# Optimization experiments

Hardware: AMD Instinct MI355X
Metric: run time of the kernel (lower is better)

Reference implementation:

```python
import jax, jax.numpy as jnp
import numpy as np

H = 16  # hidden/input size
EPS = 1e-5


def _lstm_layer(xs, W_ih, W_hh, b_ih, b_hh):
    """xs: [T, B, in]. Returns (ys [T,B,H], h_final [B,H]). PyTorch gate order i,f,g,o."""
    B = xs.shape[1]
    h0 = jnp.zeros((B, H), xs.dtype)
    c0 = jnp.zeros((B, H), xs.dtype)
    bias = b_ih + b_hh  # [4H]

    def step(carry, x_t):
        h, c = carry
        gates = x_t @ W_ih.T + h @ W_hh.T + bias  # [B, 4H]
        i, f, g, o = jnp.split(gates, 4, axis=-1)
        i = jax.nn.sigmoid(i)
        f = jax.nn.sigmoid(f)
        g = jnp.tanh(g)
        o = jax.nn.sigmoid(o)
        c = f * c + i * g
        h = o * jnp.tanh(c)
        return (h, c), h

    (h_fin, _), ys = jax.lax.scan(step, (h0, c0), xs)
    return ys, h_fin


def setup_inputs() -> dict:
    key = jax.random.key(0)
    ks = jax.random.split(key, 12)
    s = 1.0 / np.sqrt(H)  # PyTorch LSTM/Linear init scale
    B, T = 4096, 512
    x = jax.random.normal(ks[0], (B, T, H), dtype=jnp.float32)
    u = lambda k, shp: jax.random.uniform(k, shp, jnp.float32, -s, s)
    return {
        "x": x,
        "W_ih0": u(ks[1], (4 * H, H)), "W_hh0": u(ks[2], (4 * H, H)),
        "b_ih0": u(ks[3], (4 * H,)), "b_hh0": u(ks[4], (4 * H,)),
        "W_ih1": u(ks[5], (4 * H, H)), "W_hh1": u(ks[6], (4 * H, H)),
        "b_ih1": u(ks[7], (4 * H,)), "b_hh1": u(ks[8], (4 * H,)),
        "W_proj": u(ks[9], (H, H)), "b_proj": u(ks[10], (H,)),
        "ln_gamma": jnp.ones((H,), jnp.float32), "ln_beta": jnp.zeros((H,), jnp.float32),
    }


def reference(x, W_ih0, W_hh0, b_ih0, b_hh0, W_ih1, W_hh1, b_ih1, b_hh1,
              W_proj, b_proj, ln_gamma, ln_beta):
    xs = jnp.transpose(x, (1, 0, 2))  # [T, B, H] time-major for scan
    ys, _ = _lstm_layer(xs, W_ih0, W_hh0, b_ih0, b_hh0)
    _, h_n = _lstm_layer(ys, W_ih1, W_hh1, b_ih1, b_hh1)  # h_n[-1] == layer-2 final h
    z = h_n @ W_proj.T + b_proj  # [B, H]
    mu = jnp.mean(z, axis=-1, keepdims=True)
    var = jnp.mean(jnp.square(z - mu), axis=-1, keepdims=True)
    z = (z - mu) * jax.lax.rsqrt(var + EPS) * ln_gamma + ln_beta
    return jnp.tanh(z)
```

## Files before the change

### kernel.cpp

```cpp
#include <hip/hip_runtime.h>
#include <cstddef>

#define HH 16
#define TT 512
#define STG 16
#define LOG2E 1.44269504088896340736f

typedef float v2f __attribute__((ext_vector_type(2)));
typedef float v4f __attribute__((ext_vector_type(4)));

static __device__ __forceinline__ float fexp2(float x){ return __builtin_amdgcn_exp2f(x); }
static __device__ __forceinline__ float frcp (float x){ return __builtin_amdgcn_rcpf(x); }
static __device__ __forceinline__ float frsq (float x){ return __builtin_amdgcn_rsqf(x); }

static __device__ __forceinline__ float ftanh(float c){
    return frcp(1.0f + fexp2(c * (-2.0f*LOG2E))) * 2.0f - 1.0f;
}

template<int CTRL>
static __device__ __forceinline__ float qb(float v){
    return __builtin_bit_cast(float,
        __builtin_amdgcn_update_dpp(0, __builtin_bit_cast(int,v), CTRL, 0xF, 0xF, true));
}

static __device__ __forceinline__ v2f pkfma(v2f a, v2f b, v2f c){
    return __builtin_elementwise_fma(a, b, c);
}

static __device__ __forceinline__ float dot16v(const v4f* a, const v4f* w){
    v2f s0 = {0.f, 0.f}, s1 = {0.f, 0.f};
    s0 = pkfma(a[0].lo, w[0].lo, s0);  s1 = pkfma(a[0].hi, w[0].hi, s1);
    s0 = pkfma(a[1].lo, w[1].lo, s0);  s1 = pkfma(a[1].hi, w[1].hi, s1);
    s0 = pkfma(a[2].lo, w[2].lo, s0);  s1 = pkfma(a[2].hi, w[2].hi, s1);
    s0 = pkfma(a[3].lo, w[3].lo, s0);  s1 = pkfma(a[3].hi, w[3].hi, s1);
    v2f s = s0 + s1;
    return s.x + s.y;
}

__global__ __launch_bounds__(256, 4) void lstm_fused_kernel(
    const float* __restrict__ x,
    const float* __restrict__ W_ih0, const float* __restrict__ W_hh0,
    const float* __restrict__ b_ih0, const float* __restrict__ b_hh0,
    const float* __restrict__ W_ih1, const float* __restrict__ W_hh1,
    const float* __restrict__ b_ih1, const float* __restrict__ b_hh1,
    const float* __restrict__ W_proj, const float* __restrict__ b_proj,
    const float* __restrict__ ln_g, const float* __restrict__ ln_b,
    float* __restrict__ out)
{
    const int lane = threadIdx.x & 63;
    const int wave = threadIdx.x >> 6;
    const int b    = blockIdx.x * 4 + wave;

    const int g   = lane & 3;
    const int k   = lane >> 2;
    const int row = g * HH + k;

    __shared__ float sh[4 * 288];
    float* xw  = sh + wave * 288;
    float* h1w = xw + 256;
    float* h2w = h1w + 16;

    v4f wih0[4], whh0[4], wih1[4], whh1[4];
#pragma unroll
    for (int q = 0; q < 4; ++q) {
        wih0[q] = ((const v4f*)(W_ih0 + row * HH))[q];
        whh0[q] = ((const v4f*)(W_hh0 + row * HH))[q];
        wih1[q] = ((const v4f*)(W_ih1 + row * HH))[q];
        whh1[q] = ((const v4f*)(W_hh1 + row * HH))[q];
    }
    const float bias0 = b_ih0[row] + b_hh0[row];
    const float bias1 = b_ih1[row] + b_hh1[row];

    const bool  isg    = (g == 2);
    const float sc_in  = isg ? (-2.0f * LOG2E) : (-LOG2E);
    const float sc_out = isg ? 2.0f : 1.0f;
    const float sh_out = isg ? 1.0f : 0.0f;

    float c1 = 0.0f, c2 = 0.0f;
    v4f h1a[4], h2a[4];
#pragma unroll
    for (int q = 0; q < 4; ++q) { h1a[q] = (v4f)(0.f); h2a[q] = (v4f)(0.f); }

    const float* xb = x + (size_t)b * TT * HH;

    v4f xs = *(const v4f*)(xb + lane * 4);

    for (int t0 = 0; t0 < TT; t0 += STG) {
        *(v4f*)(xw + lane * 4) = xs;
        asm volatile("" ::: "memory");
        if (t0 + STG < TT)
            xs = *(const v4f*)(xb + (size_t)(t0 + STG) * HH + lane * 4);

#pragma unroll
        for (int ti = 0; ti < STG; ++ti) {
            v4f xa[4];
            {
                const v4f* p = (const v4f*)(xw + ti * HH);
                xa[0] = p[0]; xa[1] = p[1]; xa[2] = p[2]; xa[3] = p[3];
            }

            float a1 = bias0 + dot16v(xa, wih0) + dot16v(h1a, whh0);
            float act1 = frcp(1.0f + fexp2(a1 * sc_in)) * sc_out - sh_out;
            float i1 = qb<0x00>(act1), f1 = qb<0x55>(act1);
            float g1 = qb<0xAA>(act1), o1 = qb<0xFF>(act1);
            c1 = __builtin_fmaf(f1, c1, i1 * g1);
            float h1n = o1 * ftanh(c1);

            h1w[k] = h1n;
            asm volatile("" ::: "memory");
            {
                const v4f* p = (const v4f*)h1w;
                h1a[0] = p[0]; h1a[1] = p[1]; h1a[2] = p[2]; h1a[3] = p[3];
            }

            float a2 = bias1 + dot16v(h1a, wih1) + dot16v(h2a, whh1);
            float act2 = frcp(1.0f + fexp2(a2 * sc_in)) * sc_out - sh_out;
            float i2 = qb<0x00>(act2), f2 = qb<0x55>(act2);
            float g2 = qb<0xAA>(act2), o2 = qb<0xFF>(act2);
            c2 = __builtin_fmaf(f2, c2, i2 * g2);
            float h2n = o2 * ftanh(c2);

            h2w[k] = h2n;
            asm volatile("" ::: "memory");
            {
                const v4f* p = (const v4f*)h2w;
                h2a[0] = p[0]; h2a[1] = p[1]; h2a[2] = p[2]; h2a[3] = p[3];
            }
        }
        asm volatile("" ::: "memory");
    }

    const int u = lane & 15;
    v4f wp[4];
#pragma unroll
    for (int q = 0; q < 4; ++q) wp[q] = ((const v4f*)(W_proj + u * HH))[q];
    float z = b_proj[u] + dot16v(h2a, wp);

    float s = z;
    s += __shfl_xor(s, 1); s += __shfl_xor(s, 2);
    s += __shfl_xor(s, 4); s += __shfl_xor(s, 8);
    const float mu = s * (1.0f / 16.0f);

    const float d = z - mu;
    float q2 = d * d;
    q2 += __shfl_xor(q2, 1); q2 += __shfl_xor(q2, 2);
    q2 += __shfl_xor(q2, 4); q2 += __shfl_xor(q2, 8);
    const float var = q2 * (1.0f / 16.0f);

    const float rs  = frsq(var + 1e-5f);
    const float y   = d * rs * ln_g[u] + ln_b[u];
    const float res = ftanh(y);

    if (lane < 16) out[(size_t)b * HH + lane] = res;
}

extern "C" void kernel_launch(void* const* d_in, const int* in_sizes, int n_in,
                              void* d_out, int out_size, void* d_ws, size_t ws_size,
                              hipStream_t stream) {
    const float* x      = (const float*)d_in[0];
    const float* W_ih0  = (const float*)d_in[1];
    const float* W_hh0  = (const float*)d_in[2];
    const float* b_ih0  = (const float*)d_in[3];
    const float* b_hh0  = (const float*)d_in[4];
    const float* W_ih1  = (const float*)d_in[5];
    const float* W_hh1  = (const float*)d_in[6];
    const float* b_ih1  = (const float*)d_in[7];
    const float* b_hh1  = (const float*)d_in[8];
    const float* W_proj = (const float*)d_in[9];
    const float* b_proj = (const float*)d_in[10];
    const float* ln_g   = (const float*)d_in[11];
    const float* ln_b   = (const float*)d_in[12];
    float* out = (float*)d_out;

    const int B = in_sizes[0] / (TT * HH);
    dim3 grid(B / 4), block(256);
    hipLaunchKernelGGL(lstm_fused_kernel, grid, block, 0, stream,
                       x, W_ih0, W_hh0, b_ih0, b_hh0,
                       W_ih1, W_hh1, b_ih1, b_hh1,
                       W_proj, b_proj, ln_g, ln_b, out);
}
```

Baseline: 513.4 us.

## Skew LSTM layer 1 one step ahead and double-buffer x staging

```diff
diff --git a/kernel.cpp b/kernel.cpp
--- a/kernel.cpp
+++ b/kernel.cpp
@@ -4,6 +4,7 @@
 #define HH 16
 #define TT 512
 #define STG 16
+#define NSTG (TT / STG)
 #define LOG2E 1.44269504088896340736f
 
 typedef float v2f __attribute__((ext_vector_type(2)));
@@ -27,14 +28,16 @@
     return __builtin_elementwise_fma(a, b, c);
 }
 
-static __device__ __forceinline__ float dot16v(const v4f* a, const v4f* w){
-    v2f s0 = {0.f, 0.f}, s1 = {0.f, 0.f};
+static __device__ __forceinline__ void dot16_acc(const v4f* a, const v4f* w, v2f& s0, v2f& s1){
     s0 = pkfma(a[0].lo, w[0].lo, s0);  s1 = pkfma(a[0].hi, w[0].hi, s1);
     s0 = pkfma(a[1].lo, w[1].lo, s0);  s1 = pkfma(a[1].hi, w[1].hi, s1);
     s0 = pkfma(a[2].lo, w[2].lo, s0);  s1 = pkfma(a[2].hi, w[2].hi, s1);
     s0 = pkfma(a[3].lo, w[3].lo, s0);  s1 = pkfma(a[3].hi, w[3].hi, s1);
-    v2f s = s0 + s1;
-    return s.x + s.y;
+}
+
+static __device__ __forceinline__ void ld4(v4f* dst, const float* p){
+    const v4f* q = (const v4f*)p;
+    dst[0] = q[0]; dst[1] = q[1]; dst[2] = q[2]; dst[3] = q[3];
 }
 
 __global__ __launch_bounds__(256, 4) void lstm_fused_kernel(
@@ -55,9 +58,10 @@
     const int k   = lane >> 2;
     const int row = g * HH + k;
 
-    __shared__ float sh[4 * 288];
-    float* xw  = sh + wave * 288;
-    float* h1w = xw + 256;
+    __shared__ float sh[4 * 544];
+    float* xb0 = sh + wave * 544;
+    float* xb1 = xb0 + 256;
+    float* h1w = xb1 + 256;
     float* h2w = h1w + 16;
 
     v4f wih0[4], whh0[4], wih1[4], whh1[4];
@@ -76,70 +80,88 @@
     const float sc_out = isg ? 2.0f : 1.0f;
     const float sh_out = isg ? 1.0f : 0.0f;
 
-    float c1 = 0.0f, c2 = 0.0f;
+    const float* xg = x + (size_t)b * TT * HH;
+
+    v4f xs = *(const v4f*)(xg + lane * 4);
+    *(v4f*)(xb0 + lane * 4) = xs;
+    xs = *(const v4f*)(xg + 256 + lane * 4);
+
+    v4f xa[4];
+    ld4(xa, xb0);
+
+    float c1, c2 = 0.0f;
     v4f h1a[4], h2a[4];
 #pragma unroll
-    for (int q = 0; q < 4; ++q) { h1a[q] = (v4f)(0.f); h2a[q] = (v4f)(0.f); }
-
-    const float* xb = x + (size_t)b * TT * HH;
-
-    v4f xs = *(const v4f*)(xb + lane * 4);
-
-    for (int t0 = 0; t0 < TT; t0 += STG) {
-        *(v4f*)(xw + lane * 4) = xs;
-        asm volatile("" ::: "memory");
-        if (t0 + STG < TT)
-            xs = *(const v4f*)(xb + (size_t)(t0 + STG) * HH + lane * 4);
+    for (int q = 0; q < 4; ++q) h2a[q] = (v4f)(0.f);
+
+    {
+        v2f p0 = {bias0, 0.f}, p1 = {0.f, 0.f};
+        dot16_acc(xa, wih0, p0, p1);
+        v2f ps = p0 + p1;
+        float a1 = ps.x + ps.y;
+        float act1 = frcp(1.0f + fexp2(a1 * sc_in)) * sc_out - sh_out;
+        float i1 = qb<0x00>(act1), g1 = qb<0xAA>(act1), o1 = qb<0xFF>(act1);
+        c1 = i1 * g1;
+        float h1n = o1 * ftanh(c1);
+        h1w[k] = h1n;
+        ld4(h1a, h1w);
+        ld4(xa, xb0 + HH);
+    }
+
+    for (int s = 0; s < NSTG; ++s) {
+        float* cur = (s & 1) ? xb1 : xb0;
+        float* nxt = (s & 1) ? xb0 : xb1;
+
+        *(v4f*)(nxt + lane * 4) = xs;
+        const int sp = (s + 2 < NSTG) ? (s + 2) : (NSTG - 1);
+        xs = *(const v4f*)(xg + (size_t)sp * 256 + lane * 4);
 
 #pragma unroll
         for (int ti = 0; ti < STG; ++ti) {
-            v4f xa[4];
-            {
-                const v4f* p = (const v4f*)(xw + ti * HH);
-                xa[0] = p[0]; xa[1] = p[1]; xa[2] = p[2]; xa[3] = p[3];
-            }
-
-            float a1 = bias0 + dot16v(xa, wih0) + dot16v(h1a, whh0);
+            v2f p0 = {bias0, 0.f}, p1 = {0.f, 0.f};
+            dot16_acc(xa, wih0, p0, p1);
+            dot16_acc(h1a, whh0, p0, p1);
+            v2f ps = p0 + p1;
+            float a1 = ps.x + ps.y;
             float act1 = frcp(1.0f + fexp2(a1 * sc_in)) * sc_out - sh_out;
             float i1 = qb<0x00>(act1), f1 = qb<0x55>(act1);
             float g1 = qb<0xAA>(act1), o1 = qb<0xFF>(act1);
             c1 = __builtin_fmaf(f1, c1, i1 * g1);
             float h1n = o1 * ftanh(c1);
-
             h1w[k] = h1n;
-            asm volatile("" ::: "memory");
-            {
-                const v4f* p = (const v4f*)h1w;
-                h1a[0] = p[0]; h1a[1] = p[1]; h1a[2] = p[2]; h1a[3] = p[3];
-            }
-
-            float a2 = bias1 + dot16v(h1a, wih1) + dot16v(h2a, whh1);
+
+            v2f q0 = {bias1, 0.f}, q1 = {0.f, 0.f};
+            dot16_acc(h1a, wih1, q0, q1);
+
+            ld4(h1a, h1w);
+            ld4(xa, (ti <= 13) ? (cur + (ti + 2) * HH) : (nxt + (ti - 14) * HH));
+
+            dot16_acc(h2a, whh1, q0, q1);
+            v2f qs = q0 + q1;
+            float a2 = qs.x + qs.y;
             float act2 = frcp(1.0f + fexp2(a2 * sc_in)) * sc_out - sh_out;
             float i2 = qb<0x00>(act2), f2 = qb<0x55>(act2);
             float g2 = qb<0xAA>(act2), o2 = qb<0xFF>(act2);
             c2 = __builtin_fmaf(f2, c2, i2 * g2);
             float h2n = o2 * ftanh(c2);
-
             h2w[k] = h2n;
-            asm volatile("" ::: "memory");
-            {
-                const v4f* p = (const v4f*)h2w;
-                h2a[0] = p[0]; h2a[1] = p[1]; h2a[2] = p[2]; h2a[3] = p[3];
-            }
+            ld4(h2a, h2w);
         }
-        asm volatile("" ::: "memory");
     }
 
     const int u = lane & 15;
     v4f wp[4];
 #pragma unroll
     for (int q = 0; q < 4; ++q) wp[q] = ((const v4f*)(W_proj + u * HH))[q];
-    float z = b_proj[u] + dot16v(h2a, wp);
-
-    float s = z;
-    s += __shfl_xor(s, 1); s += __shfl_xor(s, 2);
-    s += __shfl_xor(s, 4); s += __shfl_xor(s, 8);
-    const float mu = s * (1.0f / 16.0f);
+    v2f z0 = {0.f, 0.f}, z1 = {0.f, 0.f};
+    dot16_acc(h2a, wp, z0, z1);
+    v2f zs = z0 + z1;
+    float z = b_proj[u] + zs.x + zs.y;
+
+    float sacc = z;
+    sacc += __shfl_xor(sacc, 1); sacc += __shfl_xor(sacc, 2);
+    sacc += __shfl_xor(sacc, 4); sacc += __shfl_xor(sacc, 8);
+    const float mu = sacc * (1.0f / 16.0f);
 
     const float d = z - mu;
     float q2 = d * d;
```

Result: faster. 491.6 us (-4.3%).
